# Kernel optimization log

Measured on AMD Instinct MI355X. Metric: run time of the kernel, lower is better.

Reference implementation:

```python
import jax, jax.numpy as jnp
import numpy as np

IN, HID, NCLS = 16, 50, 20


def setup_inputs() -> dict:
    key = jax.random.key(0)
    ks = jax.random.split(key, 7)
    B, T = 8192, 128
    s_ih = 1.0 / np.sqrt(HID)
    return {
        "x": jax.random.normal(ks[0], (B, T, IN), dtype=jnp.float32),
        # PyTorch LSTM params, gate order (i, f, g, o)
        "W_ih": jax.random.uniform(ks[1], (4 * HID, IN), jnp.float32, -s_ih, s_ih),
        "W_hh": jax.random.uniform(ks[2], (4 * HID, HID), jnp.float32, -s_ih, s_ih),
        "b_ih": jax.random.uniform(ks[3], (4 * HID,), jnp.float32, -s_ih, s_ih),
        "b_hh": jax.random.uniform(ks[4], (4 * HID,), jnp.float32, -s_ih, s_ih),
        "W_fc": jax.random.uniform(ks[5], (NCLS, HID), jnp.float32, -s_ih, s_ih),
        "b_fc": jax.random.uniform(ks[6], (NCLS,), jnp.float32, -s_ih, s_ih),
    }


def _lstm_last_hidden(x, W_ih, W_hh, b_ih, b_hh):
    # x: [B, T, IN] -> precompute input projections for all steps: [T, B, 4H]
    B = x.shape[0]
    xg = jnp.einsum("bti,gi->tbg", x, W_ih) + (b_ih + b_hh)

    def step(carry, xg_t):
        h, c = carry
        gates = xg_t + h @ W_hh.T  # [B, 4H]
        i, f, g, o = jnp.split(gates, 4, axis=-1)
        i = jax.nn.sigmoid(i)
        f = jax.nn.sigmoid(f)
        g = jnp.tanh(g)
        o = jax.nn.sigmoid(o)
        c = f * c + i * g
        h = o * jnp.tanh(c)
        return (h, c), None

    h0 = jnp.zeros((B, HID), x.dtype)
    c0 = jnp.zeros((B, HID), x.dtype)
    (hT, _), _ = jax.lax.scan(step, (h0, c0), xg)
    return hT  # == out[:, -1, :]


def reference(x, W_ih, W_hh, b_ih, b_hh, W_fc, b_fc):
    hT = _lstm_last_hidden(x.astype(jnp.float32), W_ih, W_hh, b_ih, b_hh)
    # dropout is identity in eval mode; relu then linear head on last timestep
    feat = jax.nn.relu(hT)
    logits = feat @ W_fc.T + b_fc  # [B, NCLS]
    return logits
```

## Files before the change

kernel.cpp:

```cpp
#include <hip/hip_runtime.h>

#define IN_    16
#define HID_   50
#define T_     128
#define NCLS_  20
#define BPB_   16
#define NTHR_  320
#define KP_    104
#define KPW_   52

typedef _Float16 half8 __attribute__((ext_vector_type(8)));
typedef float    f32x4 __attribute__((ext_vector_type(4)));
typedef unsigned int u32;

#define L2E_ 1.4426950408889634f
__device__ __forceinline__ u32 pkh2(float a, float b) {
    union { u32 v; _Float16 h[2]; } p; p.h[0] = (_Float16)a; p.h[1] = (_Float16)b; return p.v;
}
#define MFMA(A, B, C) __builtin_amdgcn_mfma_f32_16x16x32_f16((A), (B), (C), 0, 0, 0)
#define SIGS(v)  __builtin_amdgcn_rcpf(1.0f + __builtin_amdgcn_exp2f(v))
#define TANHS(v) fmaf(2.0f, __builtin_amdgcn_rcpf(1.0f + __builtin_amdgcn_exp2f(v)), -1.0f)

__device__ __forceinline__ half8 load_afrag(const float* __restrict__ W_ih,
                                            const float* __restrict__ W_hh,
                                            const float* __restrict__ b_ih,
                                            const float* __restrict__ b_hh,
                                            int s, int c, int q) {
    half8 r = {};
    const int u = s >> 2, kk = s & 3;
    if (u < HID_) {
        const float sc = (kk == 2) ? (-2.0f * L2E_) : (-L2E_);
        const int g = kk * HID_ + u;
        #pragma unroll
        for (int e = 0; e < 8; ++e) {
            const int k = c * 32 + q * 8 + e;
            float w = 0.f;
            if (k < IN_)                 w = W_ih[g * IN_ + k];
            else if (k < IN_ + HID_)     w = W_hh[g * HID_ + (k - IN_)];
            else if (k == IN_ + HID_)    w = b_ih[g] + b_hh[g];
            r[e] = (_Float16)(w * sc);
        }
    }
    return r;
}

__global__ __launch_bounds__(NTHR_, 6)
void lstm_mfma(const float* __restrict__ x,
               const float* __restrict__ W_ih,
               const float* __restrict__ W_hh,
               const float* __restrict__ b_ih,
               const float* __restrict__ b_hh,
               const float* __restrict__ W_fc,
               const float* __restrict__ b_fc,
               float* __restrict__ out)
{
    __shared__ __align__(16) _Float16 st[2][BPB_ * KP_];

    const int tid  = threadIdx.x;
    const int lane = tid & 63;
    const int wv   = tid >> 6;
    const int b0   = blockIdx.x * BPB_;
    const bool comp = (wv < 4);

    for (int idx = tid; idx < 2 * BPB_ * KPW_; idx += NTHR_)
        ((u32*)st)[idx] = ((idx % KPW_) == 33) ? 0x00003C00u : 0u;

    const int q    = lane >> 4;
    const int bcol = lane & 15;
    const int brow = bcol * KP_ + q * 8;

    const int t0 = comp ? (3 * wv) : 12;
    const int s0 = t0 * 16 + (lane & 15);
    half8 A00 = {}, A01 = {}, A02 = {};
    half8 A10 = {}, A11 = {}, A12 = {};
    half8 A20 = {}, A21 = {}, A22 = {};
    A00 = load_afrag(W_ih, W_hh, b_ih, b_hh, s0, 0, q);
    A01 = load_afrag(W_ih, W_hh, b_ih, b_hh, s0, 1, q);
    A02 = load_afrag(W_ih, W_hh, b_ih, b_hh, s0, 2, q);
    if (comp) {
        A10 = load_afrag(W_ih, W_hh, b_ih, b_hh, s0 + 16, 0, q);
        A11 = load_afrag(W_ih, W_hh, b_ih, b_hh, s0 + 16, 1, q);
        A12 = load_afrag(W_ih, W_hh, b_ih, b_hh, s0 + 16, 2, q);
        A20 = load_afrag(W_ih, W_hh, b_ih, b_hh, s0 + 32, 0, q);
        A21 = load_afrag(W_ih, W_hh, b_ih, b_hh, s0 + 32, 1, q);
        A22 = load_afrag(W_ih, W_hh, b_ih, b_hh, s0 + 32, 2, q);
    }

    const int u0 = t0 * 4 + q;
    const int u1 = u0 + 4;
    const int u2 = u0 + 8;
    float c0_ = 0.f, c1_ = 0.f, c2_ = 0.f;

    const int hrow0 = bcol * KP_ + IN_ + u0;
    const int hrow1 = bcol * KP_ + IN_ + u1;
    const int hrow2 = bcol * KP_ + IN_ + u2;

    const int lb = lane >> 2, fq = lane & 3;
    const float* xq = x + (size_t)(b0 + lb) * (T_ * IN_) + 4 * fq;
    const int xo = lb * KPW_ + 2 * fq;

    float4 xr = {0.f, 0.f, 0.f, 0.f};
    __syncthreads();
    if (!comp) {
        const float4 v = *(const float4*)xq;
        u32* d = (u32*)st[0];
        d[xo] = pkh2(v.x, v.y); d[xo + 1] = pkh2(v.z, v.w);
        xr = *(const float4*)(xq + IN_);
    }
    __syncthreads();

    for (int t = 0; t < T_; ++t) {
        const _Float16* sc = st[t & 1];
        _Float16*       sn = st[(t & 1) ^ 1];

        const half8 B0 = *(const half8*)(sc + brow);
        const half8 B1 = *(const half8*)(sc + brow + 32);
        const half8 B2 = *(const half8*)(sc + brow + 64);
        const f32x4 Z = {0.f, 0.f, 0.f, 0.f};

        if (comp) {
            f32x4 C0 = MFMA(A00, B0, Z);
            f32x4 C1 = MFMA(A10, B0, Z);
            f32x4 C2 = MFMA(A20, B0, Z);
            C0 = MFMA(A01, B1, C0);
            C1 = MFMA(A11, B1, C1);
            C2 = MFMA(A21, B1, C2);
            C0 = MFMA(A02, B2, C0);
            C1 = MFMA(A12, B2, C1);
            C2 = MFMA(A22, B2, C2);

            {   const float iv = SIGS(C0[0]), fv = SIGS(C0[1]);
                const float gv = TANHS(C0[2]), ov = SIGS(C0[3]);
                c0_ = fmaf(fv, c0_, iv * gv);
                sn[hrow0] = (_Float16)(ov * TANHS(c0_ * (-2.0f * L2E_))); }
            {   const float iv = SIGS(C1[0]), fv = SIGS(C1[1]);
                const float gv = TANHS(C1[2]), ov = SIGS(C1[3]);
                c1_ = fmaf(fv, c1_, iv * gv);
                sn[hrow1] = (_Float16)(ov * TANHS(c1_ * (-2.0f * L2E_))); }
            {   const float iv = SIGS(C2[0]), fv = SIGS(C2[1]);
                const float gv = TANHS(C2[2]), ov = SIGS(C2[3]);
                c2_ = fmaf(fv, c2_, iv * gv);
                sn[hrow2] = (_Float16)(ov * TANHS(c2_ * (-2.0f * L2E_))); }
        } else {
            f32x4 C0 = MFMA(A00, B0, Z);
            C0 = MFMA(A01, B1, C0);
            C0 = MFMA(A02, B2, C0);
            const float iv = SIGS(C0[0]), fv = SIGS(C0[1]);
            const float gv = TANHS(C0[2]), ov = SIGS(C0[3]);
            c0_ = fmaf(fv, c0_, iv * gv);
            if (u0 < HID_) sn[hrow0] = (_Float16)(ov * TANHS(c0_ * (-2.0f * L2E_)));
            if (t + 1 < T_) {
                u32* d = (u32*)sn;
                d[xo] = pkh2(xr.x, xr.y); d[xo + 1] = pkh2(xr.z, xr.w);
            }
            if (t + 2 < T_) xr = *(const float4*)(xq + (size_t)(t + 2) * IN_);
        }
        __syncthreads();
    }

    const _Float16* hf = st[0];

    {
        const int b  = tid / NCLS_;
        const int cl = tid - b * NCLS_;
        float acc = b_fc[cl];
        #pragma unroll
        for (int j = 0; j < HID_; ++j) {
            const float hv = fmaxf((float)hf[b * KP_ + IN_ + j], 0.0f);
            acc = fmaf(hv, W_fc[cl * HID_ + j], acc);
        }
        out[(size_t)(b0 + b) * NCLS_ + cl] = acc;
    }
}

extern "C" void kernel_launch(void* const* d_in, const int* in_sizes, int n_in,
                              void* d_out, int out_size, void* d_ws, size_t ws_size,
                              hipStream_t stream) {
    const float* x    = (const float*)d_in[0];
    const float* W_ih = (const float*)d_in[1];
    const float* W_hh = (const float*)d_in[2];
    const float* b_ih = (const float*)d_in[3];
    const float* b_hh = (const float*)d_in[4];
    const float* W_fc = (const float*)d_in[5];
    const float* b_fc = (const float*)d_in[6];
    float* out = (float*)d_out;

    const int B = in_sizes[0] / (T_ * IN_);
    dim3 grid(B / BPB_), block(NTHR_);
    hipLaunchKernelGGL(lstm_mfma, grid, block, 0, stream,
                       x, W_ih, W_hh, b_ih, b_hh, W_fc, b_fc, out);
}
```

Before: 92.39 us.

## Preload all timestep inputs into LDS and rebalance gate tiles across waves

Before the recurrence starts, the kernel copies the block's whole input sequence into dynamic shared memory as fp16. Each step's first MFMA operand now reads x directly from that buffer. This removes the dedicated loader wave and its per-step global loads and packed stores. The 13 gate tiles are spread 3/3/3/2/2 across the five waves, and the hidden-state stride shrinks. The cost is about 70KB of LDS per block, which lowers occupancy, plus an upfront global load that no longer overlaps with computation.

```diff
diff --git a/kernel.cpp b/kernel.cpp
--- a/kernel.cpp
+++ b/kernel.cpp
@@ -6,8 +6,12 @@
 #define NCLS_  20
 #define BPB_   16
 #define NTHR_  320
-#define KP_    104
-#define KPW_   52
+#define KP_    72
+#define KPW_   36
+#define XT_    256
+#define XALL_  (T_ * XT_)
+#define STSZ_  (BPB_ * KP_)
+#define LDSB_  ((XALL_ + 2 * STSZ_) * 2)
 
 typedef _Float16 half8 __attribute__((ext_vector_type(8)));
 typedef float    f32x4 __attribute__((ext_vector_type(4)));
@@ -54,119 +58,112 @@
                const float* __restrict__ b_fc,
                float* __restrict__ out)
 {
-    __shared__ __align__(16) _Float16 st[2][BPB_ * KP_];
+    extern __shared__ _Float16 dyn[];
+    _Float16* xall = dyn;
+    _Float16* st0  = dyn + XALL_;
+    _Float16* st1  = st0 + STSZ_;
 
     const int tid  = threadIdx.x;
     const int lane = tid & 63;
     const int wv   = tid >> 6;
     const int b0   = blockIdx.x * BPB_;
-    const bool comp = (wv < 4);
 
     for (int idx = tid; idx < 2 * BPB_ * KPW_; idx += NTHR_)
-        ((u32*)st)[idx] = ((idx % KPW_) == 33) ? 0x00003C00u : 0u;
+        ((u32*)st0)[idx] = ((idx % KPW_) == 25) ? 0x00003C00u : 0u;
 
-    const int q    = lane >> 4;
-    const int bcol = lane & 15;
-    const int brow = bcol * KP_ + q * 8;
+    for (int idx = tid; idx < T_ * BPB_ * 4; idx += NTHR_) {
+        const int tt = idx >> 6;
+        const int bb = (idx >> 2) & 15;
+        const int fq = idx & 3;
+        const float4 v = *(const float4*)(x + (size_t)(b0 + bb) * (T_ * IN_)
+                                            + (size_t)tt * IN_ + fq * 4);
+        u32* d = (u32*)(xall + tt * XT_ + bb * 16 + fq * 4);
+        d[0] = pkh2(v.x, v.y);
+        d[1] = pkh2(v.z, v.w);
+    }
 
-    const int t0 = comp ? (3 * wv) : 12;
-    const int s0 = t0 * 16 + (lane & 15);
-    half8 A00 = {}, A01 = {}, A02 = {};
-    half8 A10 = {}, A11 = {}, A12 = {};
+    const int nt    = (wv < 3) ? 3 : 2;
+    const int tile0 = (wv < 3) ? 3 * wv : 9 + 2 * (wv - 3);
+    const int q     = lane >> 4;
+    const int m     = lane & 15;
+    const int bcol  = lane & 15;
+
+    const int s0 = tile0 * 16 + m;
+    half8 A00 = load_afrag(W_ih, W_hh, b_ih, b_hh, s0,      0, q);
+    half8 A01 = load_afrag(W_ih, W_hh, b_ih, b_hh, s0,      1, q);
+    half8 A02 = load_afrag(W_ih, W_hh, b_ih, b_hh, s0,      2, q);
+    half8 A10 = load_afrag(W_ih, W_hh, b_ih, b_hh, s0 + 16, 0, q);
+    half8 A11 = load_afrag(W_ih, W_hh, b_ih, b_hh, s0 + 16, 1, q);
+    half8 A12 = load_afrag(W_ih, W_hh, b_ih, b_hh, s0 + 16, 2, q);
     half8 A20 = {}, A21 = {}, A22 = {};
-    A00 = load_afrag(W_ih, W_hh, b_ih, b_hh, s0, 0, q);
-    A01 = load_afrag(W_ih, W_hh, b_ih, b_hh, s0, 1, q);
-    A02 = load_afrag(W_ih, W_hh, b_ih, b_hh, s0, 2, q);
-    if (comp) {
-        A10 = load_afrag(W_ih, W_hh, b_ih, b_hh, s0 + 16, 0, q);
-        A11 = load_afrag(W_ih, W_hh, b_ih, b_hh, s0 + 16, 1, q);
-        A12 = load_afrag(W_ih, W_hh, b_ih, b_hh, s0 + 16, 2, q);
+    if (nt == 3) {
         A20 = load_afrag(W_ih, W_hh, b_ih, b_hh, s0 + 32, 0, q);
         A21 = load_afrag(W_ih, W_hh, b_ih, b_hh, s0 + 32, 1, q);
         A22 = load_afrag(W_ih, W_hh, b_ih, b_hh, s0 + 32, 2, q);
     }
 
-    const int u0 = t0 * 4 + q;
-    const int u1 = u0 + 4;
-    const int u2 = u0 + 8;
+    const int u0 = (tile0    ) * 4 + q;
+    const int u1 = (tile0 + 1) * 4 + q;
+    const int u2 = (tile0 + 2) * 4 + q;
     float c0_ = 0.f, c1_ = 0.f, c2_ = 0.f;
 
-    const int hrow0 = bcol * KP_ + IN_ + u0;
-    const int hrow1 = bcol * KP_ + IN_ + u1;
-    const int hrow2 = bcol * KP_ + IN_ + u2;
+    const int hrow0 = bcol * KP_ + u0;
+    const int hrow1 = bcol * KP_ + u1;
+    const int hrow2 = bcol * KP_ + u2;
 
-    const int lb = lane >> 2, fq = lane & 3;
-    const float* xq = x + (size_t)(b0 + lb) * (T_ * IN_) + 4 * fq;
-    const int xo = lb * KPW_ + 2 * fq;
+    const bool isx  = (q < 2);
+    const int xoff  = bcol * 16 + q * 8;
+    const int b0off = bcol * KP_ + (q - 2) * 8;
+    const int b1off = bcol * KP_ + 16 + q * 8;
+    const int b2off = bcol * KP_ + ((q == 0) ? 48 : 56);
 
-    float4 xr = {0.f, 0.f, 0.f, 0.f};
-    __syncthreads();
-    if (!comp) {
-        const float4 v = *(const float4*)xq;
-        u32* d = (u32*)st[0];
-        d[xo] = pkh2(v.x, v.y); d[xo + 1] = pkh2(v.z, v.w);
-        xr = *(const float4*)(xq + IN_);
-    }
     __syncthreads();
 
     for (int t = 0; t < T_; ++t) {
-        const _Float16* sc = st[t & 1];
-        _Float16*       sn = st[(t & 1) ^ 1];
+        const _Float16* sc = (t & 1) ? st1 : st0;
+        _Float16*       sn = (t & 1) ? st0 : st1;
 
-        const half8 B0 = *(const half8*)(sc + brow);
-        const half8 B1 = *(const half8*)(sc + brow + 32);
-        const half8 B2 = *(const half8*)(sc + brow + 64);
+        const _Float16* pB0 = isx ? (xall + t * XT_ + xoff) : (sc + b0off);
+        const half8 B0 = *(const half8*)pB0;
+        const half8 B1 = *(const half8*)(sc + b1off);
+        const half8 B2 = *(const half8*)(sc + b2off);
         const f32x4 Z = {0.f, 0.f, 0.f, 0.f};
 
-        if (comp) {
-            f32x4 C0 = MFMA(A00, B0, Z);
-            f32x4 C1 = MFMA(A10, B0, Z);
-            f32x4 C2 = MFMA(A20, B0, Z);
-            C0 = MFMA(A01, B1, C0);
-            C1 = MFMA(A11, B1, C1);
-            C2 = MFMA(A21, B1, C2);
-            C0 = MFMA(A02, B2, C0);
-            C1 = MFMA(A12, B2, C1);
-            C2 = MFMA(A22, B2, C2);
+        f32x4 C0 = MFMA(A00, B0, Z);
+        f32x4 C1 = MFMA(A10, B0, Z);
+        f32x4 C2 = MFMA(A20, B0, Z);
+        C0 = MFMA(A01, B1, C0);
+        C1 = MFMA(A11, B1, C1);
+        C2 = MFMA(A21, B1, C2);
+        C0 = MFMA(A02, B2, C0);
+        C1 = MFMA(A12, B2, C1);
+        C2 = MFMA(A22, B2, C2);
 
-            {   const float iv = SIGS(C0[0]), fv = SIGS(C0[1]);
-                const float gv = TANHS(C0[2]), ov = SIGS(C0[3]);
-                c0_ = fmaf(fv, c0_, iv * gv);
-                sn[hrow0] = (_Float16)(ov * TANHS(c0_ * (-2.0f * L2E_))); }
-            {   const float iv = SIGS(C1[0]), fv = SIGS(C1[1]);
-                const float gv = TANHS(C1[2]), ov = SIGS(C1[3]);
-                c1_ = fmaf(fv, c1_, iv * gv);
-                sn[hrow1] = (_Float16)(ov * TANHS(c1_ * (-2.0f * L2E_))); }
-            {   const float iv = SIGS(C2[0]), fv = SIGS(C2[1]);
-                const float gv = TANHS(C2[2]), ov = SIGS(C2[3]);
-                c2_ = fmaf(fv, c2_, iv * gv);
-                sn[hrow2] = (_Float16)(ov * TANHS(c2_ * (-2.0f * L2E_))); }
-        } else {
-            f32x4 C0 = MFMA(A00, B0, Z);
-            C0 = MFMA(A01, B1, C0);
-            C0 = MFMA(A02, B2, C0);
-            const float iv = SIGS(C0[0]), fv = SIGS(C0[1]);
+        {   const float iv = SIGS(C0[0]), fv = SIGS(C0[1]);
             const float gv = TANHS(C0[2]), ov = SIGS(C0[3]);
             c0_ = fmaf(fv, c0_, iv * gv);
-            if (u0 < HID_) sn[hrow0] = (_Float16)(ov * TANHS(c0_ * (-2.0f * L2E_)));
-            if (t + 1 < T_) {
-                u32* d = (u32*)sn;
-                d[xo] = pkh2(xr.x, xr.y); d[xo + 1] = pkh2(xr.z, xr.w);
-            }
-            if (t + 2 < T_) xr = *(const float4*)(xq + (size_t)(t + 2) * IN_);
-        }
+            if (u0 < HID_) sn[hrow0] = (_Float16)(ov * TANHS(c0_ * (-2.0f * L2E_))); }
+        {   const float iv = SIGS(C1[0]), fv = SIGS(C1[1]);
+            const float gv = TANHS(C1[2]), ov = SIGS(C1[3]);
+            c1_ = fmaf(fv, c1_, iv * gv);
+            if (u1 < HID_) sn[hrow1] = (_Float16)(ov * TANHS(c1_ * (-2.0f * L2E_))); }
+        {   const float iv = SIGS(C2[0]), fv = SIGS(C2[1]);
+            const float gv = TANHS(C2[2]), ov = SIGS(C2[3]);
+            c2_ = fmaf(fv, c2_, iv * gv);
+            if (nt == 3 && u2 < HID_)
+                sn[hrow2] = (_Float16)(ov * TANHS(c2_ * (-2.0f * L2E_))); }
+
         __syncthreads();
     }
-
-    const _Float16* hf = st[0];
 
     {
         const int b  = tid / NCLS_;
         const int cl = tid - b * NCLS_;
+        const _Float16* hf = st0 + b * KP_;
         float acc = b_fc[cl];
         #pragma unroll
         for (int j = 0; j < HID_; ++j) {
-            const float hv = fmaxf((float)hf[b * KP_ + IN_ + j], 0.0f);
+            const float hv = fmaxf((float)hf[j], 0.0f);
             acc = fmaf(hv, W_fc[cl * HID_ + j], acc);
         }
         out[(size_t)(b0 + b) * NCLS_ + cl] = acc;
@@ -185,8 +182,15 @@
     const float* b_fc = (const float*)d_in[6];
     float* out = (float*)d_out;
 
+    static bool attr_set = false;
+    if (!attr_set) {
+        hipFuncSetAttribute(reinterpret_cast<const void*>(lstm_mfma),
+                            hipFuncAttributeMaxDynamicSharedMemorySize, LDSB_);
+        attr_set = true;
+    }
+
     const int B = in_sizes[0] / (T_ * IN_);
     dim3 grid(B / BPB_), block(NTHR_);
-    hipLaunchKernelGGL(lstm_mfma, grid, block, 0, stream,
+    hipLaunchKernelGGL(lstm_mfma, grid, block, LDSB_, stream,
                        x, W_ih, W_hh, b_ih, b_hh, W_fc, b_fc, out);
 }
```

Result: slower. 118.8 us (+28.6%).

## Use four waves per block with four gate tiles per compute wave

Applied to the files above, without the earlier changes.

Reduces the block from five to four waves by having each of three compute waves handle four 16-row gate tiles instead of three, while the fourth wave keeps the last tile plus x staging. This cuts per-block wave count and barrier participants, at the cost of a longer serial MFMA/activation chain per compute wave and more registers for A fragments. Launch bounds change to four blocks per SIMD accordingly, and the FC head loops to cover all outputs with fewer threads.

```diff
diff --git a/kernel.cpp b/kernel.cpp
--- a/kernel.cpp
+++ b/kernel.cpp
@@ -5,7 +5,7 @@
 #define T_     128
 #define NCLS_  20
 #define BPB_   16
-#define NTHR_  320
+#define NTHR_  256
 #define KP_    104
 #define KPW_   52
 
@@ -44,7 +44,7 @@
     return r;
 }
 
-__global__ __launch_bounds__(NTHR_, 6)
+__global__ __launch_bounds__(NTHR_, 4)
 void lstm_mfma(const float* __restrict__ x,
                const float* __restrict__ W_ih,
                const float* __restrict__ W_hh,
@@ -60,7 +60,7 @@
     const int lane = tid & 63;
     const int wv   = tid >> 6;
     const int b0   = blockIdx.x * BPB_;
-    const bool comp = (wv < 4);
+    const bool comp = (wv < 3);
 
     for (int idx = tid; idx < 2 * BPB_ * KPW_; idx += NTHR_)
         ((u32*)st)[idx] = ((idx % KPW_) == 33) ? 0x00003C00u : 0u;
@@ -69,14 +69,13 @@
     const int bcol = lane & 15;
     const int brow = bcol * KP_ + q * 8;
 
-    const int t0 = comp ? (3 * wv) : 12;
+    const int t0 = comp ? (4 * wv) : 12;
     const int s0 = t0 * 16 + (lane & 15);
-    half8 A00 = {}, A01 = {}, A02 = {};
-    half8 A10 = {}, A11 = {}, A12 = {};
-    half8 A20 = {}, A21 = {}, A22 = {};
-    A00 = load_afrag(W_ih, W_hh, b_ih, b_hh, s0, 0, q);
-    A01 = load_afrag(W_ih, W_hh, b_ih, b_hh, s0, 1, q);
-    A02 = load_afrag(W_ih, W_hh, b_ih, b_hh, s0, 2, q);
+    half8 A00 = load_afrag(W_ih, W_hh, b_ih, b_hh, s0, 0, q);
+    half8 A01 = load_afrag(W_ih, W_hh, b_ih, b_hh, s0, 1, q);
+    half8 A02 = load_afrag(W_ih, W_hh, b_ih, b_hh, s0, 2, q);
+    half8 A10 = {}, A11 = {}, A12 = {}, A20 = {}, A21 = {}, A22 = {};
+    half8 A30 = {}, A31 = {}, A32 = {};
     if (comp) {
         A10 = load_afrag(W_ih, W_hh, b_ih, b_hh, s0 + 16, 0, q);
         A11 = load_afrag(W_ih, W_hh, b_ih, b_hh, s0 + 16, 1, q);
@@ -84,16 +83,21 @@
         A20 = load_afrag(W_ih, W_hh, b_ih, b_hh, s0 + 32, 0, q);
         A21 = load_afrag(W_ih, W_hh, b_ih, b_hh, s0 + 32, 1, q);
         A22 = load_afrag(W_ih, W_hh, b_ih, b_hh, s0 + 32, 2, q);
+        A30 = load_afrag(W_ih, W_hh, b_ih, b_hh, s0 + 48, 0, q);
+        A31 = load_afrag(W_ih, W_hh, b_ih, b_hh, s0 + 48, 1, q);
+        A32 = load_afrag(W_ih, W_hh, b_ih, b_hh, s0 + 48, 2, q);
     }
 
     const int u0 = t0 * 4 + q;
     const int u1 = u0 + 4;
     const int u2 = u0 + 8;
-    float c0_ = 0.f, c1_ = 0.f, c2_ = 0.f;
+    const int u3 = u0 + 12;
+    float c0_ = 0.f, c1_ = 0.f, c2_ = 0.f, c3_ = 0.f;
 
     const int hrow0 = bcol * KP_ + IN_ + u0;
     const int hrow1 = bcol * KP_ + IN_ + u1;
     const int hrow2 = bcol * KP_ + IN_ + u2;
+    const int hrow3 = bcol * KP_ + IN_ + u3;
 
     const int lb = lane >> 2, fq = lane & 3;
     const float* xq = x + (size_t)(b0 + lb) * (T_ * IN_) + 4 * fq;
@@ -122,12 +126,15 @@
             f32x4 C0 = MFMA(A00, B0, Z);
             f32x4 C1 = MFMA(A10, B0, Z);
             f32x4 C2 = MFMA(A20, B0, Z);
+            f32x4 C3 = MFMA(A30, B0, Z);
             C0 = MFMA(A01, B1, C0);
             C1 = MFMA(A11, B1, C1);
             C2 = MFMA(A21, B1, C2);
+            C3 = MFMA(A31, B1, C3);
             C0 = MFMA(A02, B2, C0);
             C1 = MFMA(A12, B2, C1);
             C2 = MFMA(A22, B2, C2);
+            C3 = MFMA(A32, B2, C3);
 
             {   const float iv = SIGS(C0[0]), fv = SIGS(C0[1]);
                 const float gv = TANHS(C0[2]), ov = SIGS(C0[3]);
@@ -141,6 +148,10 @@
                 const float gv = TANHS(C2[2]), ov = SIGS(C2[3]);
                 c2_ = fmaf(fv, c2_, iv * gv);
                 sn[hrow2] = (_Float16)(ov * TANHS(c2_ * (-2.0f * L2E_))); }
+            {   const float iv = SIGS(C3[0]), fv = SIGS(C3[1]);
+                const float gv = TANHS(C3[2]), ov = SIGS(C3[3]);
+                c3_ = fmaf(fv, c3_, iv * gv);
+                sn[hrow3] = (_Float16)(ov * TANHS(c3_ * (-2.0f * L2E_))); }
         } else {
             f32x4 C0 = MFMA(A00, B0, Z);
             C0 = MFMA(A01, B1, C0);
@@ -160,9 +171,9 @@
 
     const _Float16* hf = st[0];
 
-    {
-        const int b  = tid / NCLS_;
-        const int cl = tid - b * NCLS_;
+    for (int p = tid; p < BPB_ * NCLS_; p += NTHR_) {
+        const int b  = p / NCLS_;
+        const int cl = p - b * NCLS_;
         float acc = b_fc[cl];
         #pragma unroll
         for (int j = 0; j < HID_; ++j) {
```

New measurement: 96.22 us. 4.2% more time.
